# Kernel tuning notes

Hardware: AMD Instinct MI355X
Metric: run time of the kernel (lower is better)

Reference implementation:

```python
import jax, jax.numpy as jnp
import numpy as np

N = 1_000_000  # nodes
E = 4_000_000  # edges (avg degree 4)
F_IN, F_HID, F_OUT = 18, 16, 2


def setup_inputs() -> dict:
    key = jax.random.key(0)
    ks = jax.random.split(key, 6)
    x = jax.random.normal(ks[0], (N, F_IN), dtype=jnp.float32)
    edge_index = jax.random.randint(ks[1], (2, E), 0, N, dtype=jnp.int32)
    # Glorot-ish init for the two GCNConv weight matrices + zero biases (PyG default)
    W1 = jax.random.normal(ks[2], (F_IN, F_HID), dtype=jnp.float32) * (1.0 / np.sqrt(F_IN))
    b1 = jnp.zeros((F_HID,), dtype=jnp.float32)
    W2 = jax.random.normal(ks[3], (F_HID, F_OUT), dtype=jnp.float32) * (1.0 / np.sqrt(F_HID))
    b2 = jnp.zeros((F_OUT,), dtype=jnp.float32)
    return {"x": x, "W1": W1, "b1": b1, "W2": W2, "b2": b2, "edge_index": edge_index}


def reference(x, W1, b1, W2, b2, edge_index):
    n = x.shape[0]
    # PyG GCNConv: add self-loops, symmetric normalization D^-1/2 A D^-1/2
    loops = jnp.arange(n, dtype=edge_index.dtype)
    row = jnp.concatenate([edge_index[0], loops])  # source
    col = jnp.concatenate([edge_index[1], loops])  # target
    ones = jnp.ones(row.shape[0], dtype=x.dtype)
    deg = jax.ops.segment_sum(ones, col, num_segments=n)
    dis = jnp.where(deg > 0, jax.lax.rsqrt(jnp.maximum(deg, 1.0)), 0.0)
    norm = dis[row] * dis[col]  # [E+N]

    def gcn_conv(h, W, b):
        hw = h @ W                               # [N, F] small dense GEMM
        msg = hw[row] * norm[:, None]            # gather + scale  [E+N, F]
        agg = jax.ops.segment_sum(msg, col, num_segments=n)  # scatter-add
        return agg + b

    h = jax.nn.relu(gcn_conv(x, W1, b1))
    # F.dropout(training=self.training) -> identity in eval mode
    out = gcn_conv(h, W2, b2)
    return jax.nn.log_softmax(out, axis=1)
```

## Files before the change

kernel.cpp:

```cpp
#include <hip/hip_runtime.h>

#define BLK 256
#define ABLK 512
#define PBLK 512
#define PITER 32
#define EPB (PBLK * PITER)
#define F_INK 18
#define F_HIDK 16
#define CB 2048
#define CSH 11
#define MAXNC 512
#define CAPB 10240
#define SCAP CAPB

__device__ __forceinline__ unsigned f2bf(float f) {
  unsigned u = __float_as_uint(f);
  return (u + 0x7fffu + ((u >> 16) & 1u)) >> 16;
}
__device__ __forceinline__ float bflo(unsigned u) { return __uint_as_float(u << 16); }
__device__ __forceinline__ float bfhi(unsigned u) { return __uint_as_float(u & 0xffff0000u); }

__global__ __launch_bounds__(PBLK) void k_fillA(const int* __restrict__ rows,
                                                const int* __restrict__ cols,
                                                int* __restrict__ gcur,
                                                unsigned* __restrict__ epk,
                                                int e, int NC) {
  __shared__ int hist[MAXNC];
  __shared__ int cur[MAXNC];
  for (int j = threadIdx.x; j < NC; j += PBLK) hist[j] = 0;
  __syncthreads();
  const int base = blockIdx.x * EPB;
  const int4* cols4 = (const int4*)(cols + base);
  const int4* rows4 = (const int4*)(rows + base);
  int4 c4[PITER / 4], r4[PITER / 4];
#pragma unroll
  for (int k = 0; k < PITER / 4; ++k) {
    int idx = k * PBLK + threadIdx.x;
    int gi = base + idx * 4;
    if (gi + 3 < e) {
      c4[k] = cols4[idx];
      r4[k] = rows4[idx];
    } else {
      int cc[4] = {0, 0, 0, 0}, rr[4] = {0, 0, 0, 0};
      for (int j = 0; j < 4; ++j) {
        int g = gi + j;
        if (g < e) { cc[j] = cols[g]; rr[j] = rows[g]; }
        else       { cc[j] = -1; }
      }
      c4[k] = make_int4(cc[0], cc[1], cc[2], cc[3]);
      r4[k] = make_int4(rr[0], rr[1], rr[2], rr[3]);
    }
    int cc[4] = {c4[k].x, c4[k].y, c4[k].z, c4[k].w};
#pragma unroll
    for (int j = 0; j < 4; ++j)
      if (cc[j] >= 0) atomicAdd(&hist[cc[j] >> CSH], 1);
  }
  __syncthreads();
  for (int b = threadIdx.x; b < NC; b += PBLK) {
    int c = hist[b];
    int off = (c > 0) ? atomicAdd(&gcur[b], c) : 0;
    cur[b] = b * CAPB + off;
  }
  __syncthreads();
#pragma unroll
  for (int k = 0; k < PITER / 4; ++k) {
    int cc[4] = {c4[k].x, c4[k].y, c4[k].z, c4[k].w};
    int rr[4] = {r4[k].x, r4[k].y, r4[k].z, r4[k].w};
#pragma unroll
    for (int j = 0; j < 4; ++j) {
      if (cc[j] >= 0) {
        int bb = cc[j] >> CSH;
        int p = atomicAdd(&cur[bb], 1);
        if (p < (bb + 1) * CAPB)
          epk[p] = ((unsigned)(cc[j] & (CB - 1)) << 20) | (unsigned)rr[j];
      }
    }
  }
}

__global__ __launch_bounds__(PBLK) void k_sortB(const unsigned* __restrict__ epk,
                                                const int* __restrict__ gcnt,
                                                const float* __restrict__ x,
                                                const float* __restrict__ W1,
                                                unsigned* __restrict__ sorted2,
                                                int2* __restrict__ noderng,
                                                float* __restrict__ dis,
                                                uint4* __restrict__ s1b, int n) {
  __shared__ int hist[CB];
  __shared__ int psum[PBLK];
  __shared__ unsigned stage[SCAP];
  const int b = blockIdx.x;
  const int s = b * CAPB;
  const int cnt = min(gcnt[b], CAPB);
  for (int j = threadIdx.x; j < CB; j += PBLK) hist[j] = 0;
  __syncthreads();
  for (int i = threadIdx.x; i < cnt; i += PBLK)
    atomicAdd(&hist[__builtin_nontemporal_load(&epk[s + i]) >> 20], 1);
  __syncthreads();
  int loc[4];
  int sum = 0;
#pragma unroll
  for (int k = 0; k < 4; ++k) {
    int c = hist[threadIdx.x * 4 + k];
    loc[k] = sum;
    sum += c;
  }
  psum[threadIdx.x] = sum;
  __syncthreads();
  for (int off = 1; off < PBLK; off <<= 1) {
    int tv = (threadIdx.x >= off) ? psum[threadIdx.x - off] : 0;
    __syncthreads();
    psum[threadIdx.x] += tv;
    __syncthreads();
  }
  const int base0 = psum[threadIdx.x] - sum;
#pragma unroll
  for (int k = 0; k < 4; ++k) {
    int j = threadIdx.x * 4 + k;
    int bj = base0 + loc[k];
    int cj = ((k < 3) ? loc[k + 1] : sum) - loc[k];
    int node = (b << CSH) + j;
    if (node < n) {
      noderng[node] = make_int2(s + bj, s + bj + cj);
      dis[node] = rsqrtf((float)(cj + 1));
    }
    hist[j] = bj;
  }
  __syncthreads();
  for (int i = threadIdx.x; i < cnt; i += PBLK) {
    unsigned rec = epk[s + i];
    int p = atomicAdd(&hist[rec >> 20], 1);
    stage[p] = rec & 0xFFFFFu;
  }
  __syncthreads();
  for (int j = threadIdx.x; j < cnt; j += PBLK)
    sorted2[s + j] = stage[j];
  __syncthreads();
  float* xf = (float*)stage;
#pragma unroll
  for (int g = 0; g < CB / PBLK; ++g) {
    const int gbase = (b << CSH) + g * PBLK;
    if (gbase >= n) break;
    const int nrow = min(PBLK, n - gbase);
    const int lim = nrow * F_INK;
    __syncthreads();
    for (int t = threadIdx.x; t < lim; t += PBLK)
      xf[t] = x[(size_t)gbase * F_INK + t];
    __syncthreads();
    int node = gbase + (int)threadIdx.x;
    if (threadIdx.x < (unsigned)nrow) {
      float di = dis[node];
      float hw[F_HIDK];
#pragma unroll
      for (int f = 0; f < F_HIDK; ++f) hw[f] = 0.0f;
      const float* xi = &xf[threadIdx.x * F_INK];
#pragma unroll
      for (int k = 0; k < F_INK; ++k) {
        float xk = xi[k];
#pragma unroll
        for (int f = 0; f < F_HIDK; ++f) hw[f] = fmaf(xk, W1[k * F_HIDK + f], hw[f]);
      }
      unsigned w[8];
#pragma unroll
      for (int p = 0; p < 8; ++p)
        w[p] = f2bf(hw[2 * p] * di) | (f2bf(hw[2 * p + 1] * di) << 16);
      s1b[(size_t)node * 2 + 0] = make_uint4(w[0], w[1], w[2], w[3]);
      s1b[(size_t)node * 2 + 1] = make_uint4(w[4], w[5], w[6], w[7]);
    }
  }
}

#define ACC8(V)                                         \
  acc[0] += bflo(V.x); acc[1] += bfhi(V.x);             \
  acc[2] += bflo(V.y); acc[3] += bfhi(V.y);             \
  acc[4] += bflo(V.z); acc[5] += bfhi(V.z);             \
  acc[6] += bflo(V.w); acc[7] += bfhi(V.w);

__global__ __launch_bounds__(ABLK) void k_agg1(const unsigned* __restrict__ sorted2,
                                               const int2* __restrict__ noderng,
                                               const uint4* __restrict__ s1b,
                                               const float* __restrict__ dis,
                                               const float* __restrict__ b1,
                                               const float* __restrict__ W2,
                                               unsigned* __restrict__ s2b, int n) {
  const int q = threadIdx.x & 1;
  const int node = blockIdx.x * (ABLK >> 1) + (threadIdx.x >> 1);
  if (node >= n) return;
  float di = dis[node];
  uint4 sv = s1b[(size_t)node * 2 + q];
  float acc[8] = {bflo(sv.x), bfhi(sv.x), bflo(sv.y), bfhi(sv.y),
                  bflo(sv.z), bfhi(sv.z), bflo(sv.w), bfhi(sv.w)};
  int2 rng = noderng[node];
  int i = rng.x;
  const int re = rng.y;
  const int len = re - i;
  if (len > 0) {
    uint4 v0 = s1b[(size_t)sorted2[i] * 2 + q];
    if (len > 1) {
      uint4 v1 = s1b[(size_t)sorted2[i + 1] * 2 + q];
      i += 2;
      while (i < re) {
        uint4 v2 = s1b[(size_t)sorted2[i] * 2 + q];
        ACC8(v0);
        v0 = v1; v1 = v2;
        ++i;
      }
      ACC8(v0);
      v0 = v1;
    }
    ACC8(v0);
  }
  float p0 = 0.f, p1 = 0.f;
#pragma unroll
  for (int k = 0; k < 8; ++k) {
    int f = q * 8 + k;
    float h = fmaxf(fmaf(di, acc[k], b1[f]), 0.0f);
    p0 = fmaf(h, W2[f * 2 + 0], p0);
    p1 = fmaf(h, W2[f * 2 + 1], p1);
  }
  p0 += __shfl_xor(p0, 1);
  p1 += __shfl_xor(p1, 1);
  if (q == 0)
    s2b[node] = f2bf(p0 * di) | (f2bf(p1 * di) << 16);
}

__global__ __launch_bounds__(ABLK) void k_agg2(const unsigned* __restrict__ sorted2,
                                               const int2* __restrict__ noderng,
                                               const unsigned* __restrict__ s2b,
                                               const float* __restrict__ dis,
                                               const float* __restrict__ b2,
                                               float* __restrict__ out, int n) {
  const int node = blockIdx.x * ABLK + threadIdx.x;
  if (node >= n) return;
  float di = dis[node];
  unsigned sv = s2b[node];
  float a0 = bflo(sv), a1 = bfhi(sv);
  int2 rng = noderng[node];
  int i = rng.x;
  const int re = rng.y;
  const int len = re - i;
  if (len > 0) {
    unsigned v0 = s2b[sorted2[i]];
    if (len > 1) {
      unsigned v1 = s2b[sorted2[i + 1]];
      i += 2;
      while (i < re) {
        unsigned v2 = s2b[sorted2[i]];
        a0 += bflo(v0); a1 += bfhi(v0);
        v0 = v1; v1 = v2;
        ++i;
      }
      a0 += bflo(v0); a1 += bfhi(v0);
      v0 = v1;
    }
    a0 += bflo(v0); a1 += bfhi(v0);
  }
  float o0 = fmaf(di, a0, b2[0]);
  float o1 = fmaf(di, a1, b2[1]);
  float m = fmaxf(o0, o1);
  float lse = m + logf(expf(o0 - m) + expf(o1 - m));
  float2 r;
  r.x = o0 - lse;
  r.y = o1 - lse;
  ((float2*)out)[node] = r;
}

extern "C" void kernel_launch(void* const* d_in, const int* in_sizes, int n_in,
                              void* d_out, int out_size, void* d_ws, size_t ws_size,
                              hipStream_t stream) {
  const float* x  = (const float*)d_in[0];
  const float* W1 = (const float*)d_in[1];
  const float* b1 = (const float*)d_in[2];
  const float* W2 = (const float*)d_in[3];
  const float* b2 = (const float*)d_in[4];
  const int*   ei = (const int*)d_in[5];
  const int n = in_sizes[0] / F_INK;
  const int e = in_sizes[5] / 2;
  const int* rows = ei;
  const int* cols = ei + e;

  const int NC = (n + CB - 1) / CB;
  const int nblk = (e + EPB - 1) / EPB;

  char* ws = (char*)d_ws;
  size_t off = 0;
  auto alloc = [&](size_t bytes) {
    void* p = ws + off;
    off = (off + bytes + 15) & ~(size_t)15;
    return p;
  };
  float* dis        = (float*)alloc((size_t)n * 4);
  uint4* s1b        = (uint4*)alloc((size_t)n * 32);
  unsigned* s2b     = (unsigned*)alloc((size_t)n * 4);
  unsigned* epk     = (unsigned*)alloc((size_t)NC * CAPB * 4);
  unsigned* sorted2 = (unsigned*)alloc((size_t)NC * CAPB * 4);
  int2* noderng     = (int2*)alloc((size_t)n * 8);
  int* gcur         = (int*)alloc((size_t)NC * 4);
  float* outp = (float*)d_out;

  (void)hipMemsetAsync(gcur, 0, (size_t)NC * 4, stream);
  k_fillA<<<nblk, PBLK, 0, stream>>>(rows, cols, gcur, epk, e, NC);
  k_sortB<<<NC, PBLK, 0, stream>>>(epk, gcur, x, W1, sorted2, noderng, dis, s1b, n);
  k_agg1 <<<(n + (ABLK / 2) - 1) / (ABLK / 2), ABLK, 0, stream>>>(sorted2, noderng, s1b,
                                                                  dis, b1, W2, s2b, n);
  k_agg2 <<<(n + ABLK - 1) / ABLK, ABLK, 0, stream>>>(sorted2, noderng, s2b, dis, b2,
                                                      outp, n);
}
```

Baseline: 185.6 us.

## Overlap X@W1 GEMM with edge bucketing in one fused prepass kernel

Result: no change. 183.6 us (-1.1%).

```diff
diff --git a/kernel.cpp b/kernel.cpp
--- a/kernel.cpp
+++ b/kernel.cpp
@@ -1,6 +1,5 @@
 #include <hip/hip_runtime.h>
 
-#define BLK 256
 #define ABLK 512
 #define PBLK 512
 #define PITER 32
@@ -20,59 +19,97 @@
 __device__ __forceinline__ float bflo(unsigned u) { return __uint_as_float(u << 16); }
 __device__ __forceinline__ float bfhi(unsigned u) { return __uint_as_float(u & 0xffff0000u); }
 
-__global__ __launch_bounds__(PBLK) void k_fillA(const int* __restrict__ rows,
-                                                const int* __restrict__ cols,
-                                                int* __restrict__ gcur,
-                                                unsigned* __restrict__ epk,
-                                                int e, int NC) {
+__global__ __launch_bounds__(PBLK) void k_pre(const int* __restrict__ rows,
+                                              const int* __restrict__ cols,
+                                              int* __restrict__ gcur,
+                                              unsigned* __restrict__ epk,
+                                              const float* __restrict__ x,
+                                              const float* __restrict__ W1,
+                                              uint4* __restrict__ hwb,
+                                              int e, int n, int NC, int nblk) {
   __shared__ int hist[MAXNC];
   __shared__ int cur[MAXNC];
-  for (int j = threadIdx.x; j < NC; j += PBLK) hist[j] = 0;
-  __syncthreads();
-  const int base = blockIdx.x * EPB;
-  const int4* cols4 = (const int4*)(cols + base);
-  const int4* rows4 = (const int4*)(rows + base);
-  int4 c4[PITER / 4], r4[PITER / 4];
-#pragma unroll
-  for (int k = 0; k < PITER / 4; ++k) {
-    int idx = k * PBLK + threadIdx.x;
-    int gi = base + idx * 4;
-    if (gi + 3 < e) {
-      c4[k] = cols4[idx];
-      r4[k] = rows4[idx];
-    } else {
-      int cc[4] = {0, 0, 0, 0}, rr[4] = {0, 0, 0, 0};
+  __shared__ float xf[PBLK * F_INK];
+  if (blockIdx.x < nblk) {
+    for (int j = threadIdx.x; j < NC; j += PBLK) hist[j] = 0;
+    __syncthreads();
+    const int base = blockIdx.x * EPB;
+    const int4* cols4 = (const int4*)(cols + base);
+    const int4* rows4 = (const int4*)(rows + base);
+    int4 c4[PITER / 4], r4[PITER / 4];
+#pragma unroll
+    for (int k = 0; k < PITER / 4; ++k) {
+      int idx = k * PBLK + threadIdx.x;
+      int gi = base + idx * 4;
+      if (gi + 3 < e) {
+        c4[k] = cols4[idx];
+        r4[k] = rows4[idx];
+      } else {
+        int cc[4], rr[4];
+        for (int j = 0; j < 4; ++j) {
+          int g = gi + j;
+          if (g < e) { cc[j] = cols[g]; rr[j] = rows[g]; }
+          else       { cc[j] = -1; rr[j] = 0; }
+        }
+        c4[k] = make_int4(cc[0], cc[1], cc[2], cc[3]);
+        r4[k] = make_int4(rr[0], rr[1], rr[2], rr[3]);
+      }
+      int cc[4] = {c4[k].x, c4[k].y, c4[k].z, c4[k].w};
+#pragma unroll
+      for (int j = 0; j < 4; ++j)
+        if (cc[j] >= 0) atomicAdd(&hist[cc[j] >> CSH], 1);
+    }
+    __syncthreads();
+    for (int b = threadIdx.x; b < NC; b += PBLK) {
+      int c = hist[b];
+      int off = (c > 0) ? atomicAdd(&gcur[b], c) : 0;
+      cur[b] = b * CAPB + off;
+    }
+    __syncthreads();
+#pragma unroll
+    for (int k = 0; k < PITER / 4; ++k) {
+      int cc[4] = {c4[k].x, c4[k].y, c4[k].z, c4[k].w};
+      int rr[4] = {r4[k].x, r4[k].y, r4[k].z, r4[k].w};
+#pragma unroll
       for (int j = 0; j < 4; ++j) {
-        int g = gi + j;
-        if (g < e) { cc[j] = cols[g]; rr[j] = rows[g]; }
-        else       { cc[j] = -1; }
-      }
-      c4[k] = make_int4(cc[0], cc[1], cc[2], cc[3]);
-      r4[k] = make_int4(rr[0], rr[1], rr[2], rr[3]);
-    }
-    int cc[4] = {c4[k].x, c4[k].y, c4[k].z, c4[k].w};
-#pragma unroll
-    for (int j = 0; j < 4; ++j)
-      if (cc[j] >= 0) atomicAdd(&hist[cc[j] >> CSH], 1);
-  }
-  __syncthreads();
-  for (int b = threadIdx.x; b < NC; b += PBLK) {
-    int c = hist[b];
-    int off = (c > 0) ? atomicAdd(&gcur[b], c) : 0;
-    cur[b] = b * CAPB + off;
-  }
-  __syncthreads();
-#pragma unroll
-  for (int k = 0; k < PITER / 4; ++k) {
-    int cc[4] = {c4[k].x, c4[k].y, c4[k].z, c4[k].w};
-    int rr[4] = {r4[k].x, r4[k].y, r4[k].z, r4[k].w};
-#pragma unroll
-    for (int j = 0; j < 4; ++j) {
-      if (cc[j] >= 0) {
-        int bb = cc[j] >> CSH;
-        int p = atomicAdd(&cur[bb], 1);
-        if (p < (bb + 1) * CAPB)
-          epk[p] = ((unsigned)(cc[j] & (CB - 1)) << 20) | (unsigned)rr[j];
+        if (cc[j] >= 0) {
+          int bb = cc[j] >> CSH;
+          int p = atomicAdd(&cur[bb], 1);
+          if (p < (bb + 1) * CAPB)
+            epk[p] = ((unsigned)(cc[j] & (CB - 1)) << 20) | (unsigned)rr[j];
+        }
+      }
+    }
+  } else {
+    const int hb = blockIdx.x - nblk;
+#pragma unroll
+    for (int g = 0; g < CB / PBLK; ++g) {
+      const int gbase = hb * CB + g * PBLK;
+      if (gbase >= n) break;
+      const int nrow = min(PBLK, n - gbase);
+      const int lim = nrow * F_INK;
+      __syncthreads();
+      for (int t = threadIdx.x; t < lim; t += PBLK)
+        xf[t] = x[(size_t)gbase * F_INK + t];
+      __syncthreads();
+      if (threadIdx.x < (unsigned)nrow) {
+        int node = gbase + (int)threadIdx.x;
+        float hw[F_HIDK];
+#pragma unroll
+        for (int f = 0; f < F_HIDK; ++f) hw[f] = 0.0f;
+        const float* xi = &xf[threadIdx.x * F_INK];
+#pragma unroll
+        for (int k = 0; k < F_INK; ++k) {
+          float xk = xi[k];
+#pragma unroll
+          for (int f = 0; f < F_HIDK; ++f) hw[f] = fmaf(xk, W1[k * F_HIDK + f], hw[f]);
+        }
+        unsigned w[8];
+#pragma unroll
+        for (int p = 0; p < 8; ++p)
+          w[p] = f2bf(hw[2 * p]) | (f2bf(hw[2 * p + 1]) << 16);
+        hwb[(size_t)node * 2 + 0] = make_uint4(w[0], w[1], w[2], w[3]);
+        hwb[(size_t)node * 2 + 1] = make_uint4(w[4], w[5], w[6], w[7]);
       }
     }
   }
@@ -80,8 +117,7 @@
 
 __global__ __launch_bounds__(PBLK) void k_sortB(const unsigned* __restrict__ epk,
                                                 const int* __restrict__ gcnt,
-                                                const float* __restrict__ x,
-                                                const float* __restrict__ W1,
+                                                const uint4* __restrict__ hwb,
                                                 unsigned* __restrict__ sorted2,
                                                 int2* __restrict__ noderng,
                                                 float* __restrict__ dis,
@@ -94,8 +130,17 @@
   const int cnt = min(gcnt[b], CAPB);
   for (int j = threadIdx.x; j < CB; j += PBLK) hist[j] = 0;
   __syncthreads();
-  for (int i = threadIdx.x; i < cnt; i += PBLK)
-    atomicAdd(&hist[__builtin_nontemporal_load(&epk[s + i]) >> 20], 1);
+  const int cnt4 = cnt >> 2;
+  const uint4* epk4 = (const uint4*)(epk + s);
+  for (int i = threadIdx.x; i < cnt4; i += PBLK) {
+    uint4 v = epk4[i];
+    atomicAdd(&hist[v.x >> 20], 1);
+    atomicAdd(&hist[v.y >> 20], 1);
+    atomicAdd(&hist[v.z >> 20], 1);
+    atomicAdd(&hist[v.w >> 20], 1);
+  }
+  for (int i = cnt4 * 4 + threadIdx.x; i < cnt; i += PBLK)
+    atomicAdd(&hist[epk[s + i] >> 20], 1);
   __syncthreads();
   int loc[4];
   int sum = 0;
@@ -133,39 +178,27 @@
     stage[p] = rec & 0xFFFFFu;
   }
   __syncthreads();
-  for (int j = threadIdx.x; j < cnt; j += PBLK)
-    sorted2[s + j] = stage[j];
-  __syncthreads();
-  float* xf = (float*)stage;
+  uint4* so4 = (uint4*)(sorted2 + s);
+  const uint4* st4 = (const uint4*)stage;
+  for (int j = threadIdx.x; j < cnt4; j += PBLK) so4[j] = st4[j];
+  for (int j = cnt4 * 4 + threadIdx.x; j < cnt; j += PBLK) sorted2[s + j] = stage[j];
 #pragma unroll
   for (int g = 0; g < CB / PBLK; ++g) {
-    const int gbase = (b << CSH) + g * PBLK;
-    if (gbase >= n) break;
-    const int nrow = min(PBLK, n - gbase);
-    const int lim = nrow * F_INK;
-    __syncthreads();
-    for (int t = threadIdx.x; t < lim; t += PBLK)
-      xf[t] = x[(size_t)gbase * F_INK + t];
-    __syncthreads();
-    int node = gbase + (int)threadIdx.x;
-    if (threadIdx.x < (unsigned)nrow) {
+    int node = (b << CSH) + g * PBLK + (int)threadIdx.x;
+    if (node < n) {
       float di = dis[node];
-      float hw[F_HIDK];
-#pragma unroll
-      for (int f = 0; f < F_HIDK; ++f) hw[f] = 0.0f;
-      const float* xi = &xf[threadIdx.x * F_INK];
-#pragma unroll
-      for (int k = 0; k < F_INK; ++k) {
-        float xk = xi[k];
-#pragma unroll
-        for (int f = 0; f < F_HIDK; ++f) hw[f] = fmaf(xk, W1[k * F_HIDK + f], hw[f]);
-      }
-      unsigned w[8];
-#pragma unroll
-      for (int p = 0; p < 8; ++p)
-        w[p] = f2bf(hw[2 * p] * di) | (f2bf(hw[2 * p + 1] * di) << 16);
-      s1b[(size_t)node * 2 + 0] = make_uint4(w[0], w[1], w[2], w[3]);
-      s1b[(size_t)node * 2 + 1] = make_uint4(w[4], w[5], w[6], w[7]);
+      uint4 a0 = hwb[(size_t)node * 2 + 0];
+      uint4 a1 = hwb[(size_t)node * 2 + 1];
+      unsigned w0 = f2bf(bflo(a0.x) * di) | (f2bf(bfhi(a0.x) * di) << 16);
+      unsigned w1 = f2bf(bflo(a0.y) * di) | (f2bf(bfhi(a0.y) * di) << 16);
+      unsigned w2 = f2bf(bflo(a0.z) * di) | (f2bf(bfhi(a0.z) * di) << 16);
+      unsigned w3 = f2bf(bflo(a0.w) * di) | (f2bf(bfhi(a0.w) * di) << 16);
+      unsigned w4 = f2bf(bflo(a1.x) * di) | (f2bf(bfhi(a1.x) * di) << 16);
+      unsigned w5 = f2bf(bflo(a1.y) * di) | (f2bf(bfhi(a1.y) * di) << 16);
+      unsigned w6 = f2bf(bflo(a1.z) * di) | (f2bf(bfhi(a1.z) * di) << 16);
+      unsigned w7 = f2bf(bflo(a1.w) * di) | (f2bf(bfhi(a1.w) * di) << 16);
+      s1b[(size_t)node * 2 + 0] = make_uint4(w0, w1, w2, w3);
+      s1b[(size_t)node * 2 + 1] = make_uint4(w4, w5, w6, w7);
     }
   }
 }
@@ -290,6 +323,7 @@
     return p;
   };
   float* dis        = (float*)alloc((size_t)n * 4);
+  uint4* hwb        = (uint4*)alloc((size_t)n * 32);
   uint4* s1b        = (uint4*)alloc((size_t)n * 32);
   unsigned* s2b     = (unsigned*)alloc((size_t)n * 4);
   unsigned* epk     = (unsigned*)alloc((size_t)NC * CAPB * 4);
@@ -299,8 +333,9 @@
   float* outp = (float*)d_out;
 
   (void)hipMemsetAsync(gcur, 0, (size_t)NC * 4, stream);
-  k_fillA<<<nblk, PBLK, 0, stream>>>(rows, cols, gcur, epk, e, NC);
-  k_sortB<<<NC, PBLK, 0, stream>>>(epk, gcur, x, W1, sorted2, noderng, dis, s1b, n);
+  k_pre  <<<nblk + NC, PBLK, 0, stream>>>(rows, cols, gcur, epk, x, W1, hwb,
+                                          e, n, NC, nblk);
+  k_sortB<<<NC, PBLK, 0, stream>>>(epk, gcur, hwb, sorted2, noderng, dis, s1b, n);
   k_agg1 <<<(n + (ABLK / 2) - 1) / (ABLK / 2), ABLK, 0, stream>>>(sorted2, noderng, s1b,
                                                                   dis, b1, W2, s2b, n);
   k_agg2 <<<(n + ABLK - 1) / ABLK, ABLK, 0, stream>>>(sorted2, noderng, s2b, dis, b2,
```
